# Performance work log

Hardware: AMD Instinct MI355X
Metric: run time of the kernel (lower is better)

The kernel has to match this reference:

```python
import jax, jax.numpy as jnp
import numpy as np

WS = 7       # window size
HEADS = 3
DIM = 96
HEAD_DIM = DIM // HEADS
SCALE = HEAD_DIM ** -0.5


def _rel_pos_index(ws: int) -> np.ndarray:
    # Swin relative position index, flattened to (ws*ws*ws*ws,)
    coords = np.stack(np.meshgrid(np.arange(ws), np.arange(ws), indexing='ij'))  # (2,ws,ws)
    cf = coords.reshape(2, -1)                      # (2, n)
    rel = cf[:, :, None] - cf[:, None, :]           # (2, n, n)
    rel = rel.transpose(1, 2, 0).astype(np.int64)   # (n, n, 2)
    rel[:, :, 0] += ws - 1
    rel[:, :, 1] += ws - 1
    rel[:, :, 0] *= 2 * ws - 1
    return rel.sum(-1).reshape(-1)

_REL_IDX = _rel_pos_index(WS)


def setup_inputs() -> dict:
    key = jax.random.key(0)
    ks = jax.random.split(key, 6)
    return {
        'x': jax.random.normal(ks[0], (64, 56, 56, DIM), jnp.float32),
        'w_qkv': jax.random.normal(ks[1], (DIM, 3 * DIM), jnp.float32) * 0.02,
        'b_qkv': jax.random.normal(ks[2], (3 * DIM,), jnp.float32) * 0.02,
        'rel_pos': jax.random.normal(ks[3], (HEADS, (2 * WS - 1) ** 2), jnp.float32) * 0.02,
        'w_out': jax.random.normal(ks[4], (DIM, DIM), jnp.float32) * 0.02,
        'b_out': jax.random.normal(ks[5], (DIM,), jnp.float32) * 0.02,
    }


def reference(x, w_qkv, b_qkv, rel_pos, w_out, b_out):
    b, H, W, c = x.shape
    h, w = H // WS, W // WS
    n = WS * WS
    # split_into_windows: 'b (p h) (q w) c -> b h w (p q) c' (p outer -> strided windows)
    xw = x.reshape(b, WS, h, WS, w, c).transpose(0, 2, 4, 1, 3, 5).reshape(b, h, w, n, c)
    qkv = xw @ w_qkv + b_qkv                        # (b,h,w,n,3*dim)
    q, k, v = jnp.split(qkv, 3, axis=-1)

    def to_heads(t):  # (b,h,w,n,g*d) -> (b,g,h,w,n,d)
        return t.reshape(b, h, w, n, HEADS, HEAD_DIM).transpose(0, 4, 1, 2, 3, 5)

    q, k, v = to_heads(q) * SCALE, to_heads(k), to_heads(v)
    sim = jnp.einsum('bghwnd,bghwmd->bghwnm', q, k)  # (b,g,h,w,n,n)
    bias = rel_pos[:, _REL_IDX].reshape(HEADS, n, n)  # (g,n,n)
    sim = sim + bias[None, :, None, None]
    att = jax.nn.softmax(sim, axis=-1)
    out = jnp.einsum('bghwnm,bghwmd->bghwnd', att, v)
    out = out.transpose(0, 2, 3, 4, 1, 5).reshape(b, h, w, n, c)
    # merge_windows: inverse of split
    out = out.reshape(b, h, w, WS, WS, c).transpose(0, 3, 1, 4, 2, 5).reshape(b, H, W, c)
    return out @ w_out + b_out
```

## Files before the change

kernel.cpp:

```cpp
#include <hip/hip_runtime.h>
#include <math.h>

#define SCALE 0.17677669529663687f

typedef float f32x4 __attribute__((ext_vector_type(4)));
typedef short s16x8 __attribute__((ext_vector_type(8)));

__device__ __forceinline__ unsigned short f2bf(float f) {
    unsigned int u = __float_as_uint(f);
    u += 0x7fffu + ((u >> 16) & 1u);
    return (unsigned short)(u >> 16);
}
__device__ __forceinline__ float bf2f(unsigned short u) {
    return __uint_as_float((unsigned int)u << 16);
}
__device__ __forceinline__ unsigned int pk2(float a, float b) {
    return (unsigned int)f2bf(a) | ((unsigned int)f2bf(b) << 16);
}

__global__ void k_prep(const float* __restrict__ wq, const float* __restrict__ wo,
                       unsigned short* __restrict__ wqT, unsigned short* __restrict__ woT) {
    int i = blockIdx.x * 256 + threadIdx.x;
    if (i < 27648) {
        int c = i / 96, k = i - c * 96;
        float w = wq[k * 288 + c];
        if (c < 96) w *= SCALE;
        wqT[i] = f2bf(w);
    } else if (i < 36864) {
        int t = i - 27648;
        int c = t / 96, k = t - c * 96;
        woT[t] = f2bf(wo[k * 96 + c]);
    }
}

#define XSTR  104
#define QKSTR  80
#define PSTR   72

__global__ __launch_bounds__(192, 3) void k_fused(
        const float* __restrict__ x,
        const unsigned short* __restrict__ wqT,
        const float* __restrict__ b_qkv,
        const float* __restrict__ rel_pos,
        const unsigned short* __restrict__ woT,
        const float* __restrict__ b_out,
        float* __restrict__ out) {
    __shared__ unsigned short s_xb[49 * XSTR];
    __shared__ unsigned short s_u[3][4608];
    __shared__ unsigned short s_vt[3][32 * PSTR];
    __shared__ unsigned short s_relb[508];

    const int tid  = threadIdx.x;
    const int g    = tid >> 6;
    const int lane = tid & 63;
    const int ln   = lane & 15;
    const int kg   = lane >> 4;

    const int win = blockIdx.x;
    const int ww = win & 7, hh = (win >> 3) & 7, b = win >> 6;
    const size_t base = (size_t)b * 3136;

    for (int i = tid; i < 507; i += 192) s_relb[i] = f2bf(rel_pos[i]);

    for (int i = tid; i < 1176; i += 192) {
        const int tok = i / 24, c = i - tok * 24;
        const int p = tok / 7, q = tok - p * 7;
        const float4 v = *(const float4*)(x + (base + (p * 8 + hh) * 56 + q * 8 + ww) * 96 + c * 4);
        uint2 u; u.x = pk2(v.x, v.y); u.y = pk2(v.z, v.w);
        *(uint2*)(s_xb + tok * XSTR + c * 4) = u;
    }
    __syncthreads();

    unsigned short* const U  = s_u[g];
    unsigned short* const Vt = s_vt[g];

    s16x8 xf[4][3];
#pragma unroll
    for (int t = 0; t < 4; ++t) {
        int tok = 16 * t + ln; if (tok > 48) tok = 48;
#pragma unroll
        for (int ks = 0; ks < 3; ++ks)
            xf[t][ks] = *(const s16x8*)(s_xb + tok * XSTR + 32 * ks + 8 * kg);
    }

#pragma unroll
    for (int part = 0; part < 2; ++part) {
#pragma unroll
        for (int tc = 0; tc < 2; ++tc) {
            const int col = part * 96 + g * 32 + 16 * tc + ln;
            s16x8 wf[3];
#pragma unroll
            for (int ks = 0; ks < 3; ++ks)
                wf[ks] = *(const s16x8*)(wqT + (size_t)col * 96 + 32 * ks + 8 * kg);
            const float4 bs = *(const float4*)(b_qkv + part * 96 + g * 32 + 16 * tc + 4 * kg);
            const float bm = part ? 1.0f : SCALE;
#pragma unroll
            for (int tt = 0; tt < 4; ++tt) {
                f32x4 a = {bs.x * bm, bs.y * bm, bs.z * bm, bs.w * bm};
#pragma unroll
                for (int ks = 0; ks < 3; ++ks)
                    a = __builtin_amdgcn_mfma_f32_16x16x32_bf16(wf[ks], xf[tt][ks], a, 0, 0, 0);
                if (tt < 3 || ln == 0) {
                    uint2 u; u.x = pk2(a[0], a[1]); u.y = pk2(a[2], a[3]);
                    *(uint2*)(U + (16 * tt + ln) * QKSTR + part * 40 + 16 * tc + 4 * kg) = u;
                }
            }
        }
    }
#pragma unroll
    for (int tc = 0; tc < 2; ++tc) {
        const int col = 192 + g * 32 + 16 * tc + ln;
        s16x8 wf[3];
#pragma unroll
        for (int ks = 0; ks < 3; ++ks)
            wf[ks] = *(const s16x8*)(wqT + (size_t)col * 96 + 32 * ks + 8 * kg);
        const float bv = b_qkv[col];
#pragma unroll
        for (int tt = 0; tt < 4; ++tt) {
            f32x4 a = {bv, bv, bv, bv};
#pragma unroll
            for (int ks = 0; ks < 3; ++ks)
                a = __builtin_amdgcn_mfma_f32_16x16x32_bf16(xf[tt][ks], wf[ks], a, 0, 0, 0);
            uint2 u; u.x = pk2(a[0], a[1]); u.y = pk2(a[2], a[3]);
            *(uint2*)(Vt + (16 * tc + ln) * PSTR + 16 * tt + 4 * kg) = u;
        }
    }
    __syncthreads();

    s16x8 qf[4], kf[4];
#pragma unroll
    for (int t = 0; t < 4; ++t) {
        int tok = 16 * t + ln; if (tok > 48) tok = 48;
        qf[t] = *(const s16x8*)(U + tok * QKSTR + 8 * kg);
        kf[t] = *(const s16x8*)(U + tok * QKSTR + 40 + 8 * kg);
    }
    int qMap[4];
#pragma unroll
    for (int t = 0; t < 4; ++t) {
        int q = 16 * t + ln; if (q > 48) q = 48;
        qMap[t] = q + 6 * ((q * 37) >> 8) + g * 169 + 84;
    }
    int ktMap[4][4];
#pragma unroll
    for (int t = 0; t < 4; ++t)
#pragma unroll
        for (int r = 0; r < 4; ++r) {
            int kt = 16 * t + 4 * kg + r; if (kt > 48) kt = 48;
            ktMap[t][r] = kt + 6 * ((kt * 37) >> 8);
        }

#pragma unroll
    for (int th = 0; th < 2; ++th) {
        f32x4 sacc[4][2];
#pragma unroll
        for (int tk = 0; tk < 4; ++tk)
#pragma unroll
            for (int j = 0; j < 2; ++j) {
                const int tq = 2 * th + j;
                f32x4 c;
#pragma unroll
                for (int r = 0; r < 4; ++r)
                    c[r] = bf2f(s_relb[qMap[tq] - ktMap[tk][r]]);
                sacc[tk][j] = __builtin_amdgcn_mfma_f32_16x16x32_bf16(kf[tk], qf[tq], c, 0, 0, 0);
            }
#pragma unroll
        for (int j = 0; j < 2; ++j) {
            sacc[3][j][1] = -3e38f; sacc[3][j][2] = -3e38f; sacc[3][j][3] = -3e38f;
            if (kg) sacc[3][j][0] = -3e38f;
        }
#pragma unroll
        for (int j = 0; j < 2; ++j) {
            const int tq = 2 * th + j;
            float m0 = fmaxf(fmaxf(sacc[0][j][0], sacc[0][j][1]), fmaxf(sacc[0][j][2], sacc[0][j][3]));
            float m1 = fmaxf(fmaxf(sacc[1][j][0], sacc[1][j][1]), fmaxf(sacc[1][j][2], sacc[1][j][3]));
            float m2 = fmaxf(fmaxf(sacc[2][j][0], sacc[2][j][1]), fmaxf(sacc[2][j][2], sacc[2][j][3]));
            float m3 = fmaxf(fmaxf(sacc[3][j][0], sacc[3][j][1]), fmaxf(sacc[3][j][2], sacc[3][j][3]));
            float m = fmaxf(fmaxf(m0, m1), fmaxf(m2, m3));
            m = fmaxf(m, __shfl_xor(m, 16));
            m = fmaxf(m, __shfl_xor(m, 32));
            float s = 0.f;
#pragma unroll
            for (int tk = 0; tk < 4; ++tk)
#pragma unroll
                for (int r = 0; r < 4; ++r) {
                    const float e = __expf(sacc[tk][j][r] - m);
                    sacc[tk][j][r] = e; s += e;
                }
            s += __shfl_xor(s, 16);
            s += __shfl_xor(s, 32);
            const float inv = 1.0f / s;
#pragma unroll
            for (int tk = 0; tk < 4; ++tk) {
                uint2 u;
                u.x = pk2(sacc[tk][j][0] * inv, sacc[tk][j][1] * inv);
                u.y = pk2(sacc[tk][j][2] * inv, sacc[tk][j][3] * inv);
                *(uint2*)(U + (16 * tq + ln) * PSTR + 16 * tk + 4 * kg) = u;
            }
        }
    }

    s16x8 vf[2][2], pf[4][2];
#pragma unroll
    for (int td = 0; td < 2; ++td)
#pragma unroll
        for (int ks = 0; ks < 2; ++ks)
            vf[td][ks] = *(const s16x8*)(Vt + (16 * td + ln) * PSTR + 32 * ks + 8 * kg);
#pragma unroll
    for (int tq = 0; tq < 4; ++tq)
#pragma unroll
        for (int ks = 0; ks < 2; ++ks)
            pf[tq][ks] = *(const s16x8*)(U + (16 * tq + ln) * PSTR + 32 * ks + 8 * kg);
#pragma unroll
    for (int td = 0; td < 2; ++td)
#pragma unroll
        for (int tq = 0; tq < 4; ++tq) {
            f32x4 a = {0.f, 0.f, 0.f, 0.f};
            a = __builtin_amdgcn_mfma_f32_16x16x32_bf16(vf[td][0], pf[tq][0], a, 0, 0, 0);
            a = __builtin_amdgcn_mfma_f32_16x16x32_bf16(vf[td][1], pf[tq][1], a, 0, 0, 0);
            const int q = 16 * tq + ln;
            if (q < 49) {
                uint2 u; u.x = pk2(a[0], a[1]); u.y = pk2(a[2], a[3]);
                *(uint2*)(s_xb + q * XSTR + g * 32 + 16 * td + 4 * kg) = u;
            }
        }
    __syncthreads();

    s16x8 af[4][3];
#pragma unroll
    for (int tt = 0; tt < 4; ++tt) {
        int tok = 16 * tt + ln; if (tok > 48) tok = 48;
#pragma unroll
        for (int ks = 0; ks < 3; ++ks)
            af[tt][ks] = *(const s16x8*)(s_xb + tok * XSTR + 32 * ks + 8 * kg);
    }
#pragma unroll
    for (int j = 0; j < 2; ++j) {
        const int tc = 2 * g + j;
        s16x8 wf[3];
#pragma unroll
        for (int ks = 0; ks < 3; ++ks)
            wf[ks] = *(const s16x8*)(woT + (size_t)(16 * tc + ln) * 96 + 32 * ks + 8 * kg);
        const float4 bs = *(const float4*)(b_out + 16 * tc + 4 * kg);
#pragma unroll
        for (int tt = 0; tt < 4; ++tt) {
            f32x4 a = {bs.x, bs.y, bs.z, bs.w};
#pragma unroll
            for (int ks = 0; ks < 3; ++ks)
                a = __builtin_amdgcn_mfma_f32_16x16x32_bf16(wf[ks], af[tt][ks], a, 0, 0, 0);
            const int tok = 16 * tt + ln;
            if (tok < 49) {
                const int p = (tok * 37) >> 8;
                const int q = tok - p * 7;
                float4 o; o.x = a[0]; o.y = a[1]; o.z = a[2]; o.w = a[3];
                *(float4*)(out + (base + (p * 8 + hh) * 56 + q * 8 + ww) * 96 + 16 * tc + 4 * kg) = o;
            }
        }
    }
}

__global__ void winattn_fp32(const float* __restrict__ x,
                             const float* __restrict__ w_qkv,
                             const float* __restrict__ b_qkv,
                             const float* __restrict__ rel_pos,
                             const float* __restrict__ w_out,
                             const float* __restrict__ b_out,
                             float* __restrict__ out) {
    __shared__ float s_x[49][96];
    __shared__ float s_qkv[49][288];
    __shared__ float s_rel[3 * 169];
    const int t = threadIdx.x;
    const int blk = blockIdx.x;
    const int ww = blk & 7, hh = (blk >> 3) & 7, b = blk >> 6;
    for (int i = t; i < 3 * 169; i += 256) s_rel[i] = rel_pos[i];
    const float* xb = x + (size_t)b * 56 * 56 * 96;
    for (int i = t; i < 49 * 24; i += 256) {
        int tok = i / 24, ch4 = i % 24, p = tok / 7, q = tok % 7;
        float4 v = *(const float4*)(xb + (((p * 8 + hh) * 56) + (q * 8 + ww)) * 96 + ch4 * 4);
        *(float4*)(&s_x[tok][ch4 * 4]) = v;
    }
    __syncthreads();
    for (int u = t; u < 504; u += 256) {
        int cg = u % 72, rg = u / 72, col = cg * 4, r0 = rg * 7;
        float4 bq = *(const float4*)(b_qkv + col);
        float acc[7][4];
#pragma unroll
        for (int r = 0; r < 7; ++r) { acc[r][0]=bq.x; acc[r][1]=bq.y; acc[r][2]=bq.z; acc[r][3]=bq.w; }
        for (int k = 0; k < 96; k += 4) {
            float4 w0 = *(const float4*)(w_qkv + (size_t)(k+0)*288 + col);
            float4 w1 = *(const float4*)(w_qkv + (size_t)(k+1)*288 + col);
            float4 w2 = *(const float4*)(w_qkv + (size_t)(k+2)*288 + col);
            float4 w3 = *(const float4*)(w_qkv + (size_t)(k+3)*288 + col);
#pragma unroll
            for (int r = 0; r < 7; ++r) {
                float4 xv = *(const float4*)(&s_x[r0+r][k]);
                acc[r][0] += xv.x*w0.x + xv.y*w1.x + xv.z*w2.x + xv.w*w3.x;
                acc[r][1] += xv.x*w0.y + xv.y*w1.y + xv.z*w2.y + xv.w*w3.y;
                acc[r][2] += xv.x*w0.z + xv.y*w1.z + xv.z*w2.z + xv.w*w3.z;
                acc[r][3] += xv.x*w0.w + xv.y*w1.w + xv.z*w2.w + xv.w*w3.w;
            }
        }
#pragma unroll
        for (int r = 0; r < 7; ++r)
            *(float4*)(&s_qkv[r0+r][col]) = make_float4(acc[r][0],acc[r][1],acc[r][2],acc[r][3]);
    }
    __syncthreads();
    if (t < 147) {
        const int g = t / 49, qi = t - g * 49, pi = qi / 7, qq = qi - pi * 7;
        float qreg[32];
#pragma unroll
        for (int d = 0; d < 32; d += 4) {
            float4 v = *(const float4*)(&s_qkv[qi][g*32 + d]);
            qreg[d]=v.x*SCALE; qreg[d+1]=v.y*SCALE; qreg[d+2]=v.z*SCALE; qreg[d+3]=v.w*SCALE;
        }
        float sim[49]; float m = -1e30f;
        for (int j = 0; j < 49; ++j) {
            float a = 0.f;
            const float* kr = &s_qkv[j][96 + g*32];
#pragma unroll
            for (int d = 0; d < 32; d += 4) {
                float4 kv = *(const float4*)(kr + d);
                a += qreg[d]*kv.x + qreg[d+1]*kv.y + qreg[d+2]*kv.z + qreg[d+3]*kv.w;
            }
            int pj = j / 7, qj = j % 7;
            a += s_rel[g*169 + (pi-pj+6)*13 + (qq-qj+6)];
            sim[j] = a; m = fmaxf(m, a);
        }
        float s = 0.f;
        for (int j = 0; j < 49; ++j) { float e = __expf(sim[j]-m); sim[j]=e; s+=e; }
        float inv = 1.f/s;
        float o[32];
#pragma unroll
        for (int d = 0; d < 32; ++d) o[d] = 0.f;
        for (int j = 0; j < 49; ++j) {
            float p = sim[j];
            const float* vr = &s_qkv[j][192 + g*32];
#pragma unroll
            for (int d = 0; d < 32; d += 4) {
                float4 vv = *(const float4*)(vr + d);
                o[d] += p*vv.x; o[d+1] += p*vv.y; o[d+2] += p*vv.z; o[d+3] += p*vv.w;
            }
        }
#pragma unroll
        for (int d = 0; d < 32; d += 4)
            *(float4*)(&s_x[qi][g*32 + d]) = make_float4(o[d]*inv, o[d+1]*inv, o[d+2]*inv, o[d+3]*inv);
    }
    __syncthreads();
    for (int u = t; u < 336; u += 256) {
        int cg = u % 48, rg = u / 48, col = cg * 2, r0 = rg * 7;
        float b0 = b_out[col], b1 = b_out[col+1];
        float acc[7][2];
#pragma unroll
        for (int r = 0; r < 7; ++r) { acc[r][0]=b0; acc[r][1]=b1; }
        for (int k = 0; k < 96; k += 4) {
            float2 w0 = *(const float2*)(w_out + (size_t)(k+0)*96 + col);
            float2 w1 = *(const float2*)(w_out + (size_t)(k+1)*96 + col);
            float2 w2 = *(const float2*)(w_out + (size_t)(k+2)*96 + col);
            float2 w3 = *(const float2*)(w_out + (size_t)(k+3)*96 + col);
#pragma unroll
            for (int r = 0; r < 7; ++r) {
                float4 xv = *(const float4*)(&s_x[r0+r][k]);
                acc[r][0] += xv.x*w0.x + xv.y*w1.x + xv.z*w2.x + xv.w*w3.x;
                acc[r][1] += xv.x*w0.y + xv.y*w1.y + xv.z*w2.y + xv.w*w3.y;
            }
        }
#pragma unroll
        for (int r = 0; r < 7; ++r)
            *(float2*)(out + (size_t)(((b*56 + rg*8 + hh)*56) + r*8 + ww)*96 + col) =
                make_float2(acc[r][0], acc[r][1]);
    }
}

extern "C" void kernel_launch(void* const* d_in, const int* in_sizes, int n_in,
                              void* d_out, int out_size, void* d_ws, size_t ws_size,
                              hipStream_t stream) {
    const float* x       = (const float*)d_in[0];
    const float* w_qkv   = (const float*)d_in[1];
    const float* b_qkv   = (const float*)d_in[2];
    const float* rel_pos = (const float*)d_in[3];
    const float* w_out   = (const float*)d_in[4];
    const float* b_out   = (const float*)d_in[5];
    float* out = (float*)d_out;

    const size_t WQT_BYTES = (size_t)288 * 96 * 2;
    const size_t WOT_BYTES = (size_t)96 * 96 * 2;

    if (ws_size >= WQT_BYTES + WOT_BYTES) {
        unsigned short* wqT = (unsigned short*)d_ws;
        unsigned short* woT = (unsigned short*)((char*)d_ws + WQT_BYTES);
        hipLaunchKernelGGL(k_prep,  dim3(144),  dim3(256), 0, stream, w_qkv, w_out, wqT, woT);
        hipLaunchKernelGGL(k_fused, dim3(4096), dim3(192), 0, stream,
                           x, wqT, b_qkv, rel_pos, woT, b_out, out);
    } else {
        hipLaunchKernelGGL(winattn_fp32, dim3(4096), dim3(256), 0, stream,
                           x, w_qkv, b_qkv, rel_pos, w_out, b_out, out);
    }
}
```

Measured before the change: 211.0 us.

## Split each head across two waves and shrink shared memory with buffer reuse

Doubles the block from 3 to 6 waves so each head is handled by two waves, each owning half the query tiles and half the column tiles of the projections. Shared memory is cut by aliasing the V-transpose buffer onto the x staging buffer and writing attention outputs back into the per-head U buffers. Extra barriers are added to make this aliasing safe. The aim is more waves in flight per CU for better latency hiding, at the cost of more synchronisation and of each wave reloading K and the x fragments.

```diff
diff --git a/kernel.cpp b/kernel.cpp
--- a/kernel.cpp
+++ b/kernel.cpp
@@ -33,11 +33,10 @@
     }
 }
 
-#define XSTR  104
-#define QKSTR  80
-#define PSTR   72
-
-__global__ __launch_bounds__(192, 3) void k_fused(
+#define XSTR 104
+#define USTR  72
+
+__global__ __launch_bounds__(384, 6) void k_fused(
         const float* __restrict__ x,
         const unsigned short* __restrict__ wqT,
         const float* __restrict__ b_qkv,
@@ -45,13 +44,14 @@
         const unsigned short* __restrict__ woT,
         const float* __restrict__ b_out,
         float* __restrict__ out) {
-    __shared__ unsigned short s_xb[49 * XSTR];
-    __shared__ unsigned short s_u[3][4608];
-    __shared__ unsigned short s_vt[3][32 * PSTR];
+    __shared__ unsigned short s_xv[6912];
+    __shared__ unsigned short s_u[3][49 * USTR];
     __shared__ unsigned short s_relb[508];
 
     const int tid  = threadIdx.x;
-    const int g    = tid >> 6;
+    const int wv   = tid >> 6;
+    const int g    = wv >> 1;
+    const int h    = wv & 1;
     const int lane = tid & 63;
     const int ln   = lane & 15;
     const int kg   = lane >> 4;
@@ -60,19 +60,16 @@
     const int ww = win & 7, hh = (win >> 3) & 7, b = win >> 6;
     const size_t base = (size_t)b * 3136;
 
-    for (int i = tid; i < 507; i += 192) s_relb[i] = f2bf(rel_pos[i]);
-
-    for (int i = tid; i < 1176; i += 192) {
+    for (int i = tid; i < 507; i += 384) s_relb[i] = f2bf(rel_pos[i]);
+
+    for (int i = tid; i < 1176; i += 384) {
         const int tok = i / 24, c = i - tok * 24;
         const int p = tok / 7, q = tok - p * 7;
         const float4 v = *(const float4*)(x + (base + (p * 8 + hh) * 56 + q * 8 + ww) * 96 + c * 4);
         uint2 u; u.x = pk2(v.x, v.y); u.y = pk2(v.z, v.w);
-        *(uint2*)(s_xb + tok * XSTR + c * 4) = u;
-    }
-    __syncthreads();
-
-    unsigned short* const U  = s_u[g];
-    unsigned short* const Vt = s_vt[g];
+        *(uint2*)(s_xv + tok * XSTR + c * 4) = u;
+    }
+    __syncthreads();
 
     s16x8 xf[4][3];
 #pragma unroll
@@ -80,36 +77,36 @@
         int tok = 16 * t + ln; if (tok > 48) tok = 48;
 #pragma unroll
         for (int ks = 0; ks < 3; ++ks)
-            xf[t][ks] = *(const s16x8*)(s_xb + tok * XSTR + 32 * ks + 8 * kg);
-    }
+            xf[t][ks] = *(const s16x8*)(s_xv + tok * XSTR + 32 * ks + 8 * kg);
+    }
+    __syncthreads();
+
+    unsigned short* const U  = s_u[g];
+    unsigned short* const Vt = s_xv + g * (32 * USTR);
 
 #pragma unroll
     for (int part = 0; part < 2; ++part) {
-#pragma unroll
-        for (int tc = 0; tc < 2; ++tc) {
-            const int col = part * 96 + g * 32 + 16 * tc + ln;
-            s16x8 wf[3];
+        const int col = part * 96 + g * 32 + 16 * h + ln;
+        s16x8 wf[3];
+#pragma unroll
+        for (int ks = 0; ks < 3; ++ks)
+            wf[ks] = *(const s16x8*)(wqT + (size_t)col * 96 + 32 * ks + 8 * kg);
+        const float4 bs = *(const float4*)(b_qkv + part * 96 + g * 32 + 16 * h + 4 * kg);
+        const float bm = part ? 1.0f : SCALE;
+#pragma unroll
+        for (int tt = 0; tt < 4; ++tt) {
+            f32x4 a = {bs.x * bm, bs.y * bm, bs.z * bm, bs.w * bm};
 #pragma unroll
             for (int ks = 0; ks < 3; ++ks)
-                wf[ks] = *(const s16x8*)(wqT + (size_t)col * 96 + 32 * ks + 8 * kg);
-            const float4 bs = *(const float4*)(b_qkv + part * 96 + g * 32 + 16 * tc + 4 * kg);
-            const float bm = part ? 1.0f : SCALE;
-#pragma unroll
-            for (int tt = 0; tt < 4; ++tt) {
-                f32x4 a = {bs.x * bm, bs.y * bm, bs.z * bm, bs.w * bm};
-#pragma unroll
-                for (int ks = 0; ks < 3; ++ks)
-                    a = __builtin_amdgcn_mfma_f32_16x16x32_bf16(wf[ks], xf[tt][ks], a, 0, 0, 0);
-                if (tt < 3 || ln == 0) {
-                    uint2 u; u.x = pk2(a[0], a[1]); u.y = pk2(a[2], a[3]);
-                    *(uint2*)(U + (16 * tt + ln) * QKSTR + part * 40 + 16 * tc + 4 * kg) = u;
-                }
-            }
-        }
-    }
-#pragma unroll
-    for (int tc = 0; tc < 2; ++tc) {
-        const int col = 192 + g * 32 + 16 * tc + ln;
+                a = __builtin_amdgcn_mfma_f32_16x16x32_bf16(wf[ks], xf[tt][ks], a, 0, 0, 0);
+            if (tt < 3 || ln == 0) {
+                uint2 u; u.x = pk2(a[0], a[1]); u.y = pk2(a[2], a[3]);
+                *(uint2*)(U + (16 * tt + ln) * USTR + part * 40 + 16 * h + 4 * kg) = u;
+            }
+        }
+    }
+    {
+        const int col = 192 + g * 32 + 16 * h + ln;
         s16x8 wf[3];
 #pragma unroll
         for (int ks = 0; ks < 3; ++ks)
@@ -122,107 +119,108 @@
             for (int ks = 0; ks < 3; ++ks)
                 a = __builtin_amdgcn_mfma_f32_16x16x32_bf16(xf[tt][ks], wf[ks], a, 0, 0, 0);
             uint2 u; u.x = pk2(a[0], a[1]); u.y = pk2(a[2], a[3]);
-            *(uint2*)(Vt + (16 * tc + ln) * PSTR + 16 * tt + 4 * kg) = u;
-        }
-    }
-    __syncthreads();
-
-    s16x8 qf[4], kf[4];
+            *(uint2*)(Vt + (16 * h + ln) * USTR + 16 * tt + 4 * kg) = u;
+        }
+    }
+    __syncthreads();
+
+    s16x8 qf[2], kf[4];
+#pragma unroll
+    for (int j = 0; j < 2; ++j) {
+        int tok = 16 * (2 * h + j) + ln; if (tok > 48) tok = 48;
+        qf[j] = *(const s16x8*)(U + tok * USTR + 8 * kg);
+    }
 #pragma unroll
     for (int t = 0; t < 4; ++t) {
         int tok = 16 * t + ln; if (tok > 48) tok = 48;
-        qf[t] = *(const s16x8*)(U + tok * QKSTR + 8 * kg);
-        kf[t] = *(const s16x8*)(U + tok * QKSTR + 40 + 8 * kg);
-    }
-    int qMap[4];
-#pragma unroll
-    for (int t = 0; t < 4; ++t) {
-        int q = 16 * t + ln; if (q > 48) q = 48;
-        qMap[t] = q + 6 * ((q * 37) >> 8) + g * 169 + 84;
-    }
-    int ktMap[4][4];
+        kf[t] = *(const s16x8*)(U + tok * USTR + 40 + 8 * kg);
+    }
+    __syncthreads();
+
+    int qM[2];
+#pragma unroll
+    for (int j = 0; j < 2; ++j) {
+        int q = 16 * (2 * h + j) + ln; if (q > 48) q = 48;
+        qM[j] = q + 6 * ((q * 37) >> 8) + g * 169 + 84;
+    }
+    int ktM[4][4];
 #pragma unroll
     for (int t = 0; t < 4; ++t)
 #pragma unroll
         for (int r = 0; r < 4; ++r) {
             int kt = 16 * t + 4 * kg + r; if (kt > 48) kt = 48;
-            ktMap[t][r] = kt + 6 * ((kt * 37) >> 8);
-        }
-
-#pragma unroll
-    for (int th = 0; th < 2; ++th) {
-        f32x4 sacc[4][2];
+            ktM[t][r] = kt + 6 * ((kt * 37) >> 8);
+        }
+
+#pragma unroll
+    for (int j = 0; j < 2; ++j) {
+        const int tq = 2 * h + j;
+        f32x4 sacc[4];
+#pragma unroll
+        for (int tk = 0; tk < 4; ++tk) {
+            f32x4 c;
+#pragma unroll
+            for (int r = 0; r < 4; ++r)
+                c[r] = bf2f(s_relb[qM[j] - ktM[tk][r]]);
+            sacc[tk] = __builtin_amdgcn_mfma_f32_16x16x32_bf16(kf[tk], qf[j], c, 0, 0, 0);
+        }
+        sacc[3][1] = -3e38f; sacc[3][2] = -3e38f; sacc[3][3] = -3e38f;
+        if (kg) sacc[3][0] = -3e38f;
+
+        float m0 = fmaxf(fmaxf(sacc[0][0], sacc[0][1]), fmaxf(sacc[0][2], sacc[0][3]));
+        float m1 = fmaxf(fmaxf(sacc[1][0], sacc[1][1]), fmaxf(sacc[1][2], sacc[1][3]));
+        float m2 = fmaxf(fmaxf(sacc[2][0], sacc[2][1]), fmaxf(sacc[2][2], sacc[2][3]));
+        float m3 = fmaxf(fmaxf(sacc[3][0], sacc[3][1]), fmaxf(sacc[3][2], sacc[3][3]));
+        float m = fmaxf(fmaxf(m0, m1), fmaxf(m2, m3));
+        m = fmaxf(m, __shfl_xor(m, 16));
+        m = fmaxf(m, __shfl_xor(m, 32));
+        float s = 0.f;
 #pragma unroll
         for (int tk = 0; tk < 4; ++tk)
 #pragma unroll
-            for (int j = 0; j < 2; ++j) {
-                const int tq = 2 * th + j;
-                f32x4 c;
-#pragma unroll
-                for (int r = 0; r < 4; ++r)
-                    c[r] = bf2f(s_relb[qMap[tq] - ktMap[tk][r]]);
-                sacc[tk][j] = __builtin_amdgcn_mfma_f32_16x16x32_bf16(kf[tk], qf[tq], c, 0, 0, 0);
-            }
-#pragma unroll
-        for (int j = 0; j < 2; ++j) {
-            sacc[3][j][1] = -3e38f; sacc[3][j][2] = -3e38f; sacc[3][j][3] = -3e38f;
-            if (kg) sacc[3][j][0] = -3e38f;
-        }
-#pragma unroll
-        for (int j = 0; j < 2; ++j) {
-            const int tq = 2 * th + j;
-            float m0 = fmaxf(fmaxf(sacc[0][j][0], sacc[0][j][1]), fmaxf(sacc[0][j][2], sacc[0][j][3]));
-            float m1 = fmaxf(fmaxf(sacc[1][j][0], sacc[1][j][1]), fmaxf(sacc[1][j][2], sacc[1][j][3]));
-            float m2 = fmaxf(fmaxf(sacc[2][j][0], sacc[2][j][1]), fmaxf(sacc[2][j][2], sacc[2][j][3]));
-            float m3 = fmaxf(fmaxf(sacc[3][j][0], sacc[3][j][1]), fmaxf(sacc[3][j][2], sacc[3][j][3]));
-            float m = fmaxf(fmaxf(m0, m1), fmaxf(m2, m3));
-            m = fmaxf(m, __shfl_xor(m, 16));
-            m = fmaxf(m, __shfl_xor(m, 32));
-            float s = 0.f;
-#pragma unroll
-            for (int tk = 0; tk < 4; ++tk)
-#pragma unroll
-                for (int r = 0; r < 4; ++r) {
-                    const float e = __expf(sacc[tk][j][r] - m);
-                    sacc[tk][j][r] = e; s += e;
-                }
-            s += __shfl_xor(s, 16);
-            s += __shfl_xor(s, 32);
-            const float inv = 1.0f / s;
+            for (int r = 0; r < 4; ++r) {
+                const float e = __expf(sacc[tk][r] - m);
+                sacc[tk][r] = e; s += e;
+            }
+        s += __shfl_xor(s, 16);
+        s += __shfl_xor(s, 32);
+        const float inv = 1.0f / s;
+        if (tq < 3 || ln == 0) {
 #pragma unroll
             for (int tk = 0; tk < 4; ++tk) {
                 uint2 u;
-                u.x = pk2(sacc[tk][j][0] * inv, sacc[tk][j][1] * inv);
-                u.y = pk2(sacc[tk][j][2] * inv, sacc[tk][j][3] * inv);
-                *(uint2*)(U + (16 * tq + ln) * PSTR + 16 * tk + 4 * kg) = u;
-            }
-        }
-    }
-
-    s16x8 vf[2][2], pf[4][2];
-#pragma unroll
-    for (int td = 0; td < 2; ++td)
+                u.x = pk2(sacc[tk][0] * inv, sacc[tk][1] * inv);
+                u.y = pk2(sacc[tk][2] * inv, sacc[tk][3] * inv);
+                *(uint2*)(U + (16 * tq + ln) * USTR + 16 * tk + 4 * kg) = u;
+            }
+        }
+    }
+    __syncthreads();
+
+    s16x8 pf[4][2], vf[2];
+#pragma unroll
+    for (int tq = 0; tq < 4; ++tq) {
+        int pr = 16 * tq + ln; if (pr > 48) pr = 48;
 #pragma unroll
         for (int ks = 0; ks < 2; ++ks)
-            vf[td][ks] = *(const s16x8*)(Vt + (16 * td + ln) * PSTR + 32 * ks + 8 * kg);
-#pragma unroll
-    for (int tq = 0; tq < 4; ++tq)
-#pragma unroll
-        for (int ks = 0; ks < 2; ++ks)
-            pf[tq][ks] = *(const s16x8*)(U + (16 * tq + ln) * PSTR + 32 * ks + 8 * kg);
-#pragma unroll
-    for (int td = 0; td < 2; ++td)
-#pragma unroll
-        for (int tq = 0; tq < 4; ++tq) {
-            f32x4 a = {0.f, 0.f, 0.f, 0.f};
-            a = __builtin_amdgcn_mfma_f32_16x16x32_bf16(vf[td][0], pf[tq][0], a, 0, 0, 0);
-            a = __builtin_amdgcn_mfma_f32_16x16x32_bf16(vf[td][1], pf[tq][1], a, 0, 0, 0);
-            const int q = 16 * tq + ln;
-            if (q < 49) {
-                uint2 u; u.x = pk2(a[0], a[1]); u.y = pk2(a[2], a[3]);
-                *(uint2*)(s_xb + q * XSTR + g * 32 + 16 * td + 4 * kg) = u;
-            }
-        }
+            pf[tq][ks] = *(const s16x8*)(U + pr * USTR + 32 * ks + 8 * kg);
+    }
+#pragma unroll
+    for (int ks = 0; ks < 2; ++ks)
+        vf[ks] = *(const s16x8*)(Vt + (16 * h + ln) * USTR + 32 * ks + 8 * kg);
+    __syncthreads();
+
+#pragma unroll
+    for (int tq = 0; tq < 4; ++tq) {
+        f32x4 a = {0.f, 0.f, 0.f, 0.f};
+        a = __builtin_amdgcn_mfma_f32_16x16x32_bf16(vf[0], pf[tq][0], a, 0, 0, 0);
+        a = __builtin_amdgcn_mfma_f32_16x16x32_bf16(vf[1], pf[tq][1], a, 0, 0, 0);
+        const int q = 16 * tq + ln;
+        if (q < 49) {
+            uint2 u; u.x = pk2(a[0], a[1]); u.y = pk2(a[2], a[3]);
+            *(uint2*)(U + q * USTR + 16 * h + 4 * kg) = u;
+        }
+    }
     __syncthreads();
 
     s16x8 af[4][3];
@@ -231,16 +229,14 @@
         int tok = 16 * tt + ln; if (tok > 48) tok = 48;
 #pragma unroll
         for (int ks = 0; ks < 3; ++ks)
-            af[tt][ks] = *(const s16x8*)(s_xb + tok * XSTR + 32 * ks + 8 * kg);
-    }
-#pragma unroll
-    for (int j = 0; j < 2; ++j) {
-        const int tc = 2 * g + j;
+            af[tt][ks] = *(const s16x8*)(s_u[ks] + tok * USTR + 8 * kg);
+    }
+    {
         s16x8 wf[3];
 #pragma unroll
         for (int ks = 0; ks < 3; ++ks)
-            wf[ks] = *(const s16x8*)(woT + (size_t)(16 * tc + ln) * 96 + 32 * ks + 8 * kg);
-        const float4 bs = *(const float4*)(b_out + 16 * tc + 4 * kg);
+            wf[ks] = *(const s16x8*)(woT + (size_t)(16 * wv + ln) * 96 + 32 * ks + 8 * kg);
+        const float4 bs = *(const float4*)(b_out + 16 * wv + 4 * kg);
 #pragma unroll
         for (int tt = 0; tt < 4; ++tt) {
             f32x4 a = {bs.x, bs.y, bs.z, bs.w};
@@ -252,7 +248,7 @@
                 const int p = (tok * 37) >> 8;
                 const int q = tok - p * 7;
                 float4 o; o.x = a[0]; o.y = a[1]; o.z = a[2]; o.w = a[3];
-                *(float4*)(out + (base + (p * 8 + hh) * 56 + q * 8 + ww) * 96 + 16 * tc + 4 * kg) = o;
+                *(float4*)(out + (base + (p * 8 + hh) * 56 + q * 8 + ww) * 96 + 16 * wv + 4 * kg) = o;
             }
         }
     }
@@ -388,7 +384,7 @@
         unsigned short* wqT = (unsigned short*)d_ws;
         unsigned short* woT = (unsigned short*)((char*)d_ws + WQT_BYTES);
         hipLaunchKernelGGL(k_prep,  dim3(144),  dim3(256), 0, stream, w_qkv, w_out, wqT, woT);
-        hipLaunchKernelGGL(k_fused, dim3(4096), dim3(192), 0, stream,
+        hipLaunchKernelGGL(k_fused, dim3(4096), dim3(384), 0, stream,
                            x, wqT, b_qkv, rel_pos, woT, b_out, out);
     } else {
         hipLaunchKernelGGL(winattn_fp32, dim3(4096), dim3(256), 0, stream,
```

Result: slower. 257.5 us (+22.0%).

## Precompute expanded relative-position bias and shrink shared memory by aliasing buffers

Applied to the files above, without the earlier changes.

The prep kernel now expands the relative-position table into a dense per-head 49x64 fp32 bias matrix. The fused kernel loads it as float4 from global memory instead of gathering bf16 entries from shared memory with index arithmetic. Shared memory is reduced by reusing the x staging buffer for V-transpose and keeping the attention output per head in the U buffers, which removes a barrier after the QKV projection and may allow more blocks per CU. In exchange it adds a global bias read per block (cache-resident) and one extra barrier after the x fragments are loaded.

```diff
diff --git a/kernel.cpp b/kernel.cpp
--- a/kernel.cpp
+++ b/kernel.cpp
@@ -11,15 +11,14 @@
     u += 0x7fffu + ((u >> 16) & 1u);
     return (unsigned short)(u >> 16);
 }
-__device__ __forceinline__ float bf2f(unsigned short u) {
-    return __uint_as_float((unsigned int)u << 16);
-}
 __device__ __forceinline__ unsigned int pk2(float a, float b) {
     return (unsigned int)f2bf(a) | ((unsigned int)f2bf(b) << 16);
 }
 
 __global__ void k_prep(const float* __restrict__ wq, const float* __restrict__ wo,
-                       unsigned short* __restrict__ wqT, unsigned short* __restrict__ woT) {
+                       const float* __restrict__ rel_pos,
+                       unsigned short* __restrict__ wqT, unsigned short* __restrict__ woT,
+                       float* __restrict__ bias_exp) {
     int i = blockIdx.x * 256 + threadIdx.x;
     if (i < 27648) {
         int c = i / 96, k = i - c * 96;
@@ -30,25 +29,33 @@
         int t = i - 27648;
         int c = t / 96, k = t - c * 96;
         woT[t] = f2bf(wo[k * 96 + c]);
-    }
-}
-
-#define XSTR  104
-#define QKSTR  80
-#define PSTR   72
+    } else if (i < 36864 + 3 * 49 * 64) {
+        int t = i - 36864;
+        int g = t / 3136, r = t - g * 3136;
+        int q = r >> 6, kt = r & 63;
+        float v = 0.f;
+        if (kt < 49) {
+            int qp = q / 7, qq = q - qp * 7;
+            int kp = kt / 7, kq = kt - kp * 7;
+            v = rel_pos[g * 169 + (qp - kp + 6) * 13 + (qq - kq + 6)];
+        }
+        bias_exp[t] = v;
+    }
+}
+
+#define XSTR 104
+#define USTR  72
 
 __global__ __launch_bounds__(192, 3) void k_fused(
         const float* __restrict__ x,
         const unsigned short* __restrict__ wqT,
         const float* __restrict__ b_qkv,
-        const float* __restrict__ rel_pos,
+        const float* __restrict__ bias_exp,
         const unsigned short* __restrict__ woT,
         const float* __restrict__ b_out,
         float* __restrict__ out) {
-    __shared__ unsigned short s_xb[49 * XSTR];
-    __shared__ unsigned short s_u[3][4608];
-    __shared__ unsigned short s_vt[3][32 * PSTR];
-    __shared__ unsigned short s_relb[508];
+    __shared__ unsigned short s_xv[6912];
+    __shared__ unsigned short s_u[3][49 * USTR];
 
     const int tid  = threadIdx.x;
     const int g    = tid >> 6;
@@ -60,19 +67,14 @@
     const int ww = win & 7, hh = (win >> 3) & 7, b = win >> 6;
     const size_t base = (size_t)b * 3136;
 
-    for (int i = tid; i < 507; i += 192) s_relb[i] = f2bf(rel_pos[i]);
-
     for (int i = tid; i < 1176; i += 192) {
         const int tok = i / 24, c = i - tok * 24;
         const int p = tok / 7, q = tok - p * 7;
         const float4 v = *(const float4*)(x + (base + (p * 8 + hh) * 56 + q * 8 + ww) * 96 + c * 4);
         uint2 u; u.x = pk2(v.x, v.y); u.y = pk2(v.z, v.w);
-        *(uint2*)(s_xb + tok * XSTR + c * 4) = u;
-    }
-    __syncthreads();
-
-    unsigned short* const U  = s_u[g];
-    unsigned short* const Vt = s_vt[g];
+        *(uint2*)(s_xv + tok * XSTR + c * 4) = u;
+    }
+    __syncthreads();
 
     s16x8 xf[4][3];
 #pragma unroll
@@ -80,8 +82,12 @@
         int tok = 16 * t + ln; if (tok > 48) tok = 48;
 #pragma unroll
         for (int ks = 0; ks < 3; ++ks)
-            xf[t][ks] = *(const s16x8*)(s_xb + tok * XSTR + 32 * ks + 8 * kg);
-    }
+            xf[t][ks] = *(const s16x8*)(s_xv + tok * XSTR + 32 * ks + 8 * kg);
+    }
+    __syncthreads();
+
+    unsigned short* const U  = s_u[g];
+    unsigned short* const Vt = s_xv + g * (32 * USTR);
 
 #pragma unroll
     for (int part = 0; part < 2; ++part) {
@@ -102,7 +108,7 @@
                     a = __builtin_amdgcn_mfma_f32_16x16x32_bf16(wf[ks], xf[tt][ks], a, 0, 0, 0);
                 if (tt < 3 || ln == 0) {
                     uint2 u; u.x = pk2(a[0], a[1]); u.y = pk2(a[2], a[3]);
-                    *(uint2*)(U + (16 * tt + ln) * QKSTR + part * 40 + 16 * tc + 4 * kg) = u;
+                    *(uint2*)(U + (16 * tt + ln) * USTR + part * 40 + 16 * tc + 4 * kg) = u;
                 }
             }
         }
@@ -122,94 +128,78 @@
             for (int ks = 0; ks < 3; ++ks)
                 a = __builtin_amdgcn_mfma_f32_16x16x32_bf16(xf[tt][ks], wf[ks], a, 0, 0, 0);
             uint2 u; u.x = pk2(a[0], a[1]); u.y = pk2(a[2], a[3]);
-            *(uint2*)(Vt + (16 * tc + ln) * PSTR + 16 * tt + 4 * kg) = u;
-        }
-    }
-    __syncthreads();
+            *(uint2*)(Vt + (16 * tc + ln) * USTR + 16 * tt + 4 * kg) = u;
+        }
+    }
 
     s16x8 qf[4], kf[4];
 #pragma unroll
     for (int t = 0; t < 4; ++t) {
         int tok = 16 * t + ln; if (tok > 48) tok = 48;
-        qf[t] = *(const s16x8*)(U + tok * QKSTR + 8 * kg);
-        kf[t] = *(const s16x8*)(U + tok * QKSTR + 40 + 8 * kg);
-    }
-    int qMap[4];
-#pragma unroll
-    for (int t = 0; t < 4; ++t) {
-        int q = 16 * t + ln; if (q > 48) q = 48;
-        qMap[t] = q + 6 * ((q * 37) >> 8) + g * 169 + 84;
-    }
-    int ktMap[4][4];
-#pragma unroll
-    for (int t = 0; t < 4; ++t)
-#pragma unroll
-        for (int r = 0; r < 4; ++r) {
-            int kt = 16 * t + 4 * kg + r; if (kt > 48) kt = 48;
-            ktMap[t][r] = kt + 6 * ((kt * 37) >> 8);
-        }
-
-#pragma unroll
-    for (int th = 0; th < 2; ++th) {
-        f32x4 sacc[4][2];
+        qf[t] = *(const s16x8*)(U + tok * USTR + 8 * kg);
+        kf[t] = *(const s16x8*)(U + tok * USTR + 40 + 8 * kg);
+    }
+    const int qrow[4] = { ln, 16 + ln, 32 + ln, 48 };
+    f32x4 sacc[4][4];
+#pragma unroll
+    for (int tq = 0; tq < 4; ++tq) {
+        const float* brow = bias_exp + (g * 49 + qrow[tq]) * 64;
+#pragma unroll
+        for (int tk = 0; tk < 4; ++tk) {
+            const float4 bb = *(const float4*)(brow + 16 * tk + 4 * kg);
+            f32x4 c = {bb.x, bb.y, bb.z, bb.w};
+            sacc[tk][tq] = __builtin_amdgcn_mfma_f32_16x16x32_bf16(kf[tk], qf[tq], c, 0, 0, 0);
+        }
+    }
+#pragma unroll
+    for (int tq = 0; tq < 4; ++tq) {
+        sacc[3][tq][1] = -3e38f; sacc[3][tq][2] = -3e38f; sacc[3][tq][3] = -3e38f;
+        if (kg) sacc[3][tq][0] = -3e38f;
+    }
+#pragma unroll
+    for (int tq = 0; tq < 4; ++tq) {
+        float m0 = fmaxf(fmaxf(sacc[0][tq][0], sacc[0][tq][1]), fmaxf(sacc[0][tq][2], sacc[0][tq][3]));
+        float m1 = fmaxf(fmaxf(sacc[1][tq][0], sacc[1][tq][1]), fmaxf(sacc[1][tq][2], sacc[1][tq][3]));
+        float m2 = fmaxf(fmaxf(sacc[2][tq][0], sacc[2][tq][1]), fmaxf(sacc[2][tq][2], sacc[2][tq][3]));
+        float m3 = fmaxf(fmaxf(sacc[3][tq][0], sacc[3][tq][1]), fmaxf(sacc[3][tq][2], sacc[3][tq][3]));
+        float m = fmaxf(fmaxf(m0, m1), fmaxf(m2, m3));
+        m = fmaxf(m, __shfl_xor(m, 16));
+        m = fmaxf(m, __shfl_xor(m, 32));
+        float s = 0.f;
 #pragma unroll
         for (int tk = 0; tk < 4; ++tk)
 #pragma unroll
-            for (int j = 0; j < 2; ++j) {
-                const int tq = 2 * th + j;
-                f32x4 c;
-#pragma unroll
-                for (int r = 0; r < 4; ++r)
-                    c[r] = bf2f(s_relb[qMap[tq] - ktMap[tk][r]]);
-                sacc[tk][j] = __builtin_amdgcn_mfma_f32_16x16x32_bf16(kf[tk], qf[tq], c, 0, 0, 0);
-            }
-#pragma unroll
-        for (int j = 0; j < 2; ++j) {
-            sacc[3][j][1] = -3e38f; sacc[3][j][2] = -3e38f; sacc[3][j][3] = -3e38f;
-            if (kg) sacc[3][j][0] = -3e38f;
-        }
-#pragma unroll
-        for (int j = 0; j < 2; ++j) {
-            const int tq = 2 * th + j;
-            float m0 = fmaxf(fmaxf(sacc[0][j][0], sacc[0][j][1]), fmaxf(sacc[0][j][2], sacc[0][j][3]));
-            float m1 = fmaxf(fmaxf(sacc[1][j][0], sacc[1][j][1]), fmaxf(sacc[1][j][2], sacc[1][j][3]));
-            float m2 = fmaxf(fmaxf(sacc[2][j][0], sacc[2][j][1]), fmaxf(sacc[2][j][2], sacc[2][j][3]));
-            float m3 = fmaxf(fmaxf(sacc[3][j][0], sacc[3][j][1]), fmaxf(sacc[3][j][2], sacc[3][j][3]));
-            float m = fmaxf(fmaxf(m0, m1), fmaxf(m2, m3));
-            m = fmaxf(m, __shfl_xor(m, 16));
-            m = fmaxf(m, __shfl_xor(m, 32));
-            float s = 0.f;
-#pragma unroll
-            for (int tk = 0; tk < 4; ++tk)
-#pragma unroll
-                for (int r = 0; r < 4; ++r) {
-                    const float e = __expf(sacc[tk][j][r] - m);
-                    sacc[tk][j][r] = e; s += e;
-                }
-            s += __shfl_xor(s, 16);
-            s += __shfl_xor(s, 32);
-            const float inv = 1.0f / s;
+            for (int r = 0; r < 4; ++r) {
+                const float e = __expf(sacc[tk][tq][r] - m);
+                sacc[tk][tq][r] = e; s += e;
+            }
+        s += __shfl_xor(s, 16);
+        s += __shfl_xor(s, 32);
+        const float inv = 1.0f / s;
+        if (tq < 3 || ln == 0) {
 #pragma unroll
             for (int tk = 0; tk < 4; ++tk) {
                 uint2 u;
-                u.x = pk2(sacc[tk][j][0] * inv, sacc[tk][j][1] * inv);
-                u.y = pk2(sacc[tk][j][2] * inv, sacc[tk][j][3] * inv);
-                *(uint2*)(U + (16 * tq + ln) * PSTR + 16 * tk + 4 * kg) = u;
-            }
-        }
-    }
-
-    s16x8 vf[2][2], pf[4][2];
+                u.x = pk2(sacc[tk][tq][0] * inv, sacc[tk][tq][1] * inv);
+                u.y = pk2(sacc[tk][tq][2] * inv, sacc[tk][tq][3] * inv);
+                *(uint2*)(U + (16 * tq + ln) * USTR + 16 * tk + 4 * kg) = u;
+            }
+        }
+    }
+
+    s16x8 pf[4][2], vf[2][2];
+#pragma unroll
+    for (int tq = 0; tq < 4; ++tq) {
+        int pr = 16 * tq + ln; if (pr > 48) pr = 48;
+#pragma unroll
+        for (int ks = 0; ks < 2; ++ks)
+            pf[tq][ks] = *(const s16x8*)(U + pr * USTR + 32 * ks + 8 * kg);
+    }
 #pragma unroll
     for (int td = 0; td < 2; ++td)
 #pragma unroll
         for (int ks = 0; ks < 2; ++ks)
-            vf[td][ks] = *(const s16x8*)(Vt + (16 * td + ln) * PSTR + 32 * ks + 8 * kg);
-#pragma unroll
-    for (int tq = 0; tq < 4; ++tq)
-#pragma unroll
-        for (int ks = 0; ks < 2; ++ks)
-            pf[tq][ks] = *(const s16x8*)(U + (16 * tq + ln) * PSTR + 32 * ks + 8 * kg);
+            vf[td][ks] = *(const s16x8*)(Vt + (16 * td + ln) * USTR + 32 * ks + 8 * kg);
 #pragma unroll
     for (int td = 0; td < 2; ++td)
 #pragma unroll
@@ -220,7 +210,7 @@
             const int q = 16 * tq + ln;
             if (q < 49) {
                 uint2 u; u.x = pk2(a[0], a[1]); u.y = pk2(a[2], a[3]);
-                *(uint2*)(s_xb + q * XSTR + g * 32 + 16 * td + 4 * kg) = u;
+                *(uint2*)(U + q * USTR + 16 * td + 4 * kg) = u;
             }
         }
     __syncthreads();
@@ -231,7 +221,7 @@
         int tok = 16 * tt + ln; if (tok > 48) tok = 48;
 #pragma unroll
         for (int ks = 0; ks < 3; ++ks)
-            af[tt][ks] = *(const s16x8*)(s_xb + tok * XSTR + 32 * ks + 8 * kg);
+            af[tt][ks] = *(const s16x8*)(s_u[ks] + tok * USTR + 8 * kg);
     }
 #pragma unroll
     for (int j = 0; j < 2; ++j) {
@@ -381,15 +371,18 @@
     const float* b_out   = (const float*)d_in[5];
     float* out = (float*)d_out;
 
-    const size_t WQT_BYTES = (size_t)288 * 96 * 2;
-    const size_t WOT_BYTES = (size_t)96 * 96 * 2;
-
-    if (ws_size >= WQT_BYTES + WOT_BYTES) {
+    const size_t WQT_BYTES  = (size_t)288 * 96 * 2;
+    const size_t WOT_BYTES  = (size_t)96 * 96 * 2;
+    const size_t BIAS_BYTES = (size_t)3 * 49 * 64 * 4;
+
+    if (ws_size >= WQT_BYTES + WOT_BYTES + BIAS_BYTES) {
         unsigned short* wqT = (unsigned short*)d_ws;
         unsigned short* woT = (unsigned short*)((char*)d_ws + WQT_BYTES);
-        hipLaunchKernelGGL(k_prep,  dim3(144),  dim3(256), 0, stream, w_qkv, w_out, wqT, woT);
+        float* bias_exp     = (float*)((char*)d_ws + WQT_BYTES + WOT_BYTES);
+        hipLaunchKernelGGL(k_prep,  dim3(181),  dim3(256), 0, stream,
+                           w_qkv, w_out, rel_pos, wqT, woT, bias_exp);
         hipLaunchKernelGGL(k_fused, dim3(4096), dim3(192), 0, stream,
-                           x, wqT, b_qkv, rel_pos, woT, b_out, out);
+                           x, wqT, b_qkv, bias_exp, woT, b_out, out);
     } else {
         hipLaunchKernelGGL(winattn_fp32, dim3(4096), dim3(256), 0, stream,
                            x, w_qkv, b_qkv, rel_pos, w_out, b_out, out);
```

After: 200.3 us. -5.1%, faster.
